# Kernel optimization log

Measured on AMD Instinct MI355X. Metric: run time of the kernel, lower is better.

## Reference

```python
import jax, jax.numpy as jnp
import numpy as np

NUM_LAYERS = 4; HEADS = 8; DIM_HEAD = 64; DIM = 512; FF_INNER = 2048; EPS = 1e-5
B = 32; S = 512
PAGE_VOCAB = 10000; ITEM_VOCAB = 100000; META_VOCAB = 1000
N_WIDE = 8; WIDE_DIM = 64
ATTN_INNER = HEADS * DIM_HEAD
FUSED = ATTN_INNER + DIM_HEAD + DIM_HEAD + 2 * FF_INNER  # q, k, v, swiglu-ff


def rotate_half(x):
    d = x.shape[-1] // 2
    x1, x2 = x[..., :d], x[..., d:]
    return jnp.concatenate([-x2, x1], axis=-1)


def rope_pos(n, d):
    inv_freq = 1.0 / (10000.0 ** (jnp.arange(0, d, 2, dtype=jnp.float32) / d))
    freqs = jnp.arange(n, dtype=jnp.float32)[:, None] * inv_freq[None, :]
    return jnp.concatenate([freqs, freqs], axis=-1)  # (n, d)


def wide_feat(w, bn_g, bn_b, W, bvec):
    # w: (B, n_wide, S); BatchNorm1d eval mode (running mean 0, var 1) -> affine only
    wn = w * (1.0 / np.sqrt(1.0 + EPS)) * bn_g[None, :, None] + bn_b[None, :, None]
    wt = jnp.transpose(wn, (0, 2, 1))  # (B, S, n_wide)
    return jax.nn.leaky_relu(wt @ W + bvec, negative_slope=0.2)


def parallel_block(x, vl, g, Wf, Wa, Wff):
    b, n, _ = x.shape
    mu = x.mean(-1, keepdims=True)
    var = ((x - mu) ** 2).mean(-1, keepdims=True)
    xn = (x - mu) / jnp.sqrt(var + EPS) * g  # gamma-only LayerNorm
    p = xn @ Wf  # (b, n, FUSED)
    q = p[..., :ATTN_INNER]
    k = p[..., ATTN_INNER:ATTN_INNER + DIM_HEAD]
    v = p[..., ATTN_INNER + DIM_HEAD:ATTN_INNER + 2 * DIM_HEAD]
    ff = p[..., ATTN_INNER + 2 * DIM_HEAD:]
    q = jnp.transpose(q.reshape(b, n, HEADS, DIM_HEAD), (0, 2, 1, 3))  # b h n d
    pos = rope_pos(n, DIM_HEAD)
    cos, sin = jnp.cos(pos), jnp.sin(pos)
    q = q * cos + rotate_half(q) * sin
    k = k * cos + rotate_half(k) * sin  # multi-query: k,v shared across heads
    q = q * (DIM_HEAD ** -0.5)
    sim = jnp.einsum('bhid,bjd->bhij', q, k)
    key_pad = jnp.arange(n)[None, :] >= vl[:, None]  # (b, n) True = padded key
    sim = jnp.where(key_pad[:, None, None, :], -jnp.inf, sim)
    attn = jax.nn.softmax(sim, axis=-1)
    out = jnp.einsum('bhij,bjd->bhid', attn, v)
    out = jnp.transpose(out, (0, 2, 1, 3)).reshape(b, n, ATTN_INNER)
    xx, gate = ff[..., :FF_INNER], ff[..., FF_INNER:]
    return out @ Wa + (jax.nn.silu(gate) * xx) @ Wff


def forward(page_in, item_in, item_meta_in, vl_in, page_meta_in,
            page_meta_wide_in, item_meta_wide_in,
            page_emb_table, page_meta_emb_table, item_emb_table,
            item_meta_emb_table, item_pre_emb_table,
            page_wide_W, page_wide_b, page_bn_g, page_bn_b,
            item_wide_W, item_wide_b, item_bn_g, item_bn_b,
            norm_g, fused_W, attn_out_W, ff_out_W):
    page_wide = wide_feat(page_meta_wide_in, page_bn_g, page_bn_b, page_wide_W, page_wide_b)
    item_wide = wide_feat(item_meta_wide_in, item_bn_g, item_bn_b, item_wide_W, item_wide_b)
    page = jnp.concatenate([page_emb_table[page_in], page_meta_emb_table[page_meta_in], page_wide], axis=-1)
    item = jnp.concatenate([item_emb_table[item_in], item_meta_emb_table[item_meta_in],
                            item_pre_emb_table[item_in], item_wide], axis=-1)
    x = page * item  # (B, S, DIM)
    for l in range(NUM_LAYERS):
        x = parallel_block(x, vl_in, norm_g[l], fused_W[l], attn_out_W[l], ff_out_W[l]) + x
    # MeanMaxPooling (dropout=0 in eval)
    return jnp.concatenate([x.mean(axis=1), x.max(axis=1)], axis=-1)  # (B, 2*DIM)


def setup_inputs() -> dict:
    key = jax.random.key(0)
    ks = jax.random.split(key, 24)
    s = 0.02
    return {
        'page_in': jax.random.randint(ks[0], (B, S), 0, PAGE_VOCAB),
        'item_in': jax.random.randint(ks[1], (B, S), 0, ITEM_VOCAB),
        'item_meta_in': jax.random.randint(ks[2], (B, S), 0, META_VOCAB),
        'vl_in': jax.random.randint(ks[3], (B,), 1, S + 1),
        'page_meta_in': jax.random.randint(ks[4], (B, S), 0, META_VOCAB),
        'page_meta_wide_in': jax.random.normal(ks[5], (B, N_WIDE, S), jnp.float32),
        'item_meta_wide_in': jax.random.normal(ks[6], (B, N_WIDE, S), jnp.float32),
        'page_emb_table': jax.random.normal(ks[7], (PAGE_VOCAB, 384), jnp.float32) * s,
        'page_meta_emb_table': jax.random.normal(ks[8], (META_VOCAB, 64), jnp.float32) * s,
        'item_emb_table': jax.random.normal(ks[9], (ITEM_VOCAB, 320), jnp.float32) * s,
        'item_meta_emb_table': jax.random.normal(ks[10], (META_VOCAB, 64), jnp.float32) * s,
        'item_pre_emb_table': jax.random.normal(ks[11], (ITEM_VOCAB, 64), jnp.float32) * s,
        'page_wide_W': jax.random.normal(ks[12], (N_WIDE, WIDE_DIM), jnp.float32) * s,
        'page_wide_b': jnp.zeros((WIDE_DIM,), jnp.float32),
        'page_bn_g': jnp.ones((N_WIDE,), jnp.float32),
        'page_bn_b': jnp.zeros((N_WIDE,), jnp.float32),
        'item_wide_W': jax.random.normal(ks[13], (N_WIDE, WIDE_DIM), jnp.float32) * s,
        'item_wide_b': jnp.zeros((WIDE_DIM,), jnp.float32),
        'item_bn_g': jnp.ones((N_WIDE,), jnp.float32),
        'item_bn_b': jnp.zeros((N_WIDE,), jnp.float32),
        'norm_g': jnp.ones((NUM_LAYERS, DIM), jnp.float32),
        'fused_W': jax.random.normal(ks[14], (NUM_LAYERS, DIM, FUSED), jnp.float32) * s,
        'attn_out_W': jax.random.normal(ks[15], (NUM_LAYERS, ATTN_INNER, DIM), jnp.float32) * s,
        'ff_out_W': jax.random.normal(ks[16], (NUM_LAYERS, FF_INNER, DIM), jnp.float32) * s,
    }


def reference(page_in, item_in, item_meta_in, vl_in, page_meta_in,
              page_meta_wide_in, item_meta_wide_in,
              page_emb_table, page_meta_emb_table, item_emb_table,
              item_meta_emb_table, item_pre_emb_table,
              page_wide_W, page_wide_b, page_bn_g, page_bn_b,
              item_wide_W, item_wide_b, item_bn_g, item_bn_b,
              norm_g, fused_W, attn_out_W, ff_out_W):
    return forward(page_in, item_in, item_meta_in, vl_in, page_meta_in,
                   page_meta_wide_in, item_meta_wide_in,
                   page_emb_table, page_meta_emb_table, item_emb_table,
                   item_meta_emb_table, item_pre_emb_table,
                   page_wide_W, page_wide_b, page_bn_g, page_bn_b,
                   item_wide_W, item_wide_b, item_bn_g, item_bn_b,
                   norm_g, fused_W, attn_out_W, ff_out_W)
```

## Files before the change

kernel.cpp:

```cpp
#include <hip/hip_runtime.h>
#include <math.h>


namespace {
constexpr int SEQ    = 512;
constexpr int NBATCH = 32;
constexpr int DIMM   = 512;
constexpr int NHEAD  = 8;
constexpr int FFIN   = 2048;
constexpr int NFUSED = 4736;
constexpr int NROWS  = NBATCH * SEQ;
constexpr int QKVC   = 640;
}

typedef __bf16 bf16x8 __attribute__((ext_vector_type(8)));
typedef float f32x4 __attribute__((ext_vector_type(4)));
typedef unsigned short ushort8 __attribute__((ext_vector_type(8)));

static __device__ __forceinline__ unsigned short bfhi(float v, float* hf) {
    __bf16 h = (__bf16)v;
    *hf = (float)h;
    return __builtin_bit_cast(unsigned short, h);
}
static __device__ __forceinline__ unsigned short bflo(float v, float hf) {
    __bf16 l = (__bf16)(v - hf);
    return __builtin_bit_cast(unsigned short, l);
}

static __device__ __forceinline__ void gload16(const unsigned short* g,
                                               unsigned short* l) {
    __builtin_amdgcn_global_load_lds(
        (const __attribute__((address_space(1))) void*)g,
        (__attribute__((address_space(3))) void*)l,
        16, 0, 0);
}

__global__ __launch_bounds__(512) void build_x_k(
    const int* __restrict__ page_in, const int* __restrict__ item_in,
    const int* __restrict__ item_meta_in, const int* __restrict__ page_meta_in,
    const float* __restrict__ pwide, const float* __restrict__ iwide,
    const float* __restrict__ page_emb, const float* __restrict__ page_meta_emb,
    const float* __restrict__ item_emb, const float* __restrict__ item_meta_emb,
    const float* __restrict__ item_pre_emb,
    const float* __restrict__ pW, const float* __restrict__ pb,
    const float* __restrict__ pg, const float* __restrict__ pbeta,
    const float* __restrict__ iW, const float* __restrict__ ib,
    const float* __restrict__ ig, const float* __restrict__ ibeta,
    float* __restrict__ x)
{
    const int row = blockIdx.x;
    const int b = row >> 9;
    const int s = row & 511;
    const int d = threadIdx.x;
    const float BNS = 0.9999950000374997f;

    float pv, iv;
    if (d < 384) {
        pv = page_emb[(size_t)page_in[row] * 384 + d];
    } else if (d < 448) {
        pv = page_meta_emb[(size_t)page_meta_in[row] * 64 + (d - 384)];
    } else {
        const int dd = d - 448;
        float acc = pb[dd];
        #pragma unroll
        for (int c = 0; c < 8; ++c) {
            float w  = pwide[((size_t)b * 8 + c) * SEQ + s];
            float wn = w * BNS * pg[c] + pbeta[c];
            acc += wn * pW[c * 64 + dd];
        }
        pv = acc > 0.f ? acc : 0.2f * acc;
    }
    if (d < 320) {
        iv = item_emb[(size_t)item_in[row] * 320 + d];
    } else if (d < 384) {
        iv = item_meta_emb[(size_t)item_meta_in[row] * 64 + (d - 320)];
    } else if (d < 448) {
        iv = item_pre_emb[(size_t)item_in[row] * 64 + (d - 384)];
    } else {
        const int dd = d - 448;
        float acc = ib[dd];
        #pragma unroll
        for (int c = 0; c < 8; ++c) {
            float w  = iwide[((size_t)b * 8 + c) * SEQ + s];
            float wn = w * BNS * ig[c] + ibeta[c];
            acc += wn * iW[c * 64 + dd];
        }
        iv = acc > 0.f ? acc : 0.2f * acc;
    }
    x[(size_t)row * DIMM + d] = pv * iv;
}

__global__ __launch_bounds__(256) void trig_k(float* __restrict__ cost,
                                              float* __restrict__ sint)
{
    const int idx = blockIdx.x * 256 + threadIdx.x;
    const int s = idx >> 5, j = idx & 31;
    float invf = powf(10000.0f, -(float)j * (1.0f / 32.0f));
    float ang = (float)s * invf;
    float sn, cs;
    sincosf(ang, &sn, &cs);
    cost[idx] = cs;
    sint[idx] = sn;
}

__global__ __launch_bounds__(256) void ln_k(const float* __restrict__ x,
                                            unsigned short* __restrict__ xnh,
                                            const float* __restrict__ g)
{
    const int row = blockIdx.x;
    const int t = threadIdx.x;
    const float* xr = x + (size_t)row * DIMM;
    __shared__ float red[4];

    float v0 = xr[t], v1 = xr[t + 256];
    float s = v0 + v1;
    #pragma unroll
    for (int o = 32; o; o >>= 1) s += __shfl_xor(s, o);
    if ((t & 63) == 0) red[t >> 6] = s;
    __syncthreads();
    float mu = (red[0] + red[1] + red[2] + red[3]) * (1.0f / 512.0f);
    __syncthreads();

    float d0 = v0 - mu, d1 = v1 - mu;
    float vs = d0 * d0 + d1 * d1;
    #pragma unroll
    for (int o = 32; o; o >>= 1) vs += __shfl_xor(vs, o);
    if ((t & 63) == 0) red[t >> 6] = vs;
    __syncthreads();
    float var = (red[0] + red[1] + red[2] + red[3]) * (1.0f / 512.0f);
    float r = 1.0f / sqrtf(var + 1e-5f);

    const size_t base = (size_t)row * DIMM;
    float o0 = d0 * r * g[t];
    float o1 = d1 * r * g[t + 256];
    float hf;
    xnh[base + t]       = bfhi(o0, &hf);
    xnh[base + t + 256] = bfhi(o1, &hf);
}

__global__ __launch_bounds__(256) void wconv_all_k(
    const float* __restrict__ Wf, const float* __restrict__ Wa,
    const float* __restrict__ Wff,
    unsigned short* __restrict__ WqTh, unsigned short* __restrict__ WqTl,
    unsigned short* __restrict__ WdTh, unsigned short* __restrict__ WaTh,
    unsigned short* __restrict__ WfTh)
{
    __shared__ float tile[64][65];
    const int bid = blockIdx.x;
    const int t   = threadIdx.x;

    const float* W;
    unsigned short* Th;
    unsigned short* Tl = nullptr;
    int ldw, col0, ldt, nt, kt;
    bool split = false;

    if (bid < 80) {
        W = Wf; ldw = NFUSED; col0 = 0; Th = WqTh; Tl = WqTl; ldt = DIMM;
        split = true;
        nt = bid % 10; kt = bid / 10;
    } else if (bid < 592) {
        int b = bid - 80;
        W = Wf; ldw = NFUSED; col0 = 640; Th = WdTh; ldt = DIMM;
        nt = b & 63; kt = b >> 6;
    } else if (bid < 656) {
        int b = bid - 592;
        W = Wa; ldw = DIMM; col0 = 0; Th = WaTh; ldt = DIMM;
        nt = b & 7; kt = b >> 3;
    } else {
        int b = bid - 656;
        W = Wff; ldw = DIMM; col0 = 0; Th = WfTh; ldt = FFIN;
        nt = b & 7; kt = b >> 3;
    }
    nt <<= 6; kt <<= 6;

    #pragma unroll
    for (int i = 0; i < 16; ++i) {
        int flat = i * 256 + t;
        int r = flat >> 6, c = flat & 63;
        tile[r][c] = W[(size_t)(kt + r) * ldw + col0 + nt + c];
    }
    __syncthreads();
    #pragma unroll
    for (int i = 0; i < 2; ++i) {
        int flat = i * 256 + t;
        int n = flat >> 3, ck = (flat & 7) << 3;
        ushort8 hv, lv;
        #pragma unroll
        for (int j = 0; j < 8; ++j) {
            float v = tile[ck + j][n];
            float hf;
            hv[j] = bfhi(v, &hf);
            if (split) lv[j] = bflo(v, hf);
        }
        size_t o = (size_t)(nt + n) * ldt + kt + ck;
        *(ushort8*)&Th[o] = hv;
        if (split) *(ushort8*)&Tl[o] = lv;
    }
}

__global__ __launch_bounds__(256, 4) void mfma_qkv_rope_k(
    const unsigned short* __restrict__ Ah,
    const unsigned short* __restrict__ BTh, const unsigned short* __restrict__ BTl,
    const float* __restrict__ cost, const float* __restrict__ sint,
    unsigned short* __restrict__ qh,
    unsigned short* __restrict__ kh, unsigned short* __restrict__ kl,
    unsigned short* __restrict__ vT)
{
    __shared__ unsigned short smem[128 * 64 + 64 * 64 + 64 * 64];
    unsigned short* sA  = smem;
    unsigned short* sBh = smem + 128 * 64;
    unsigned short* sBl = smem + 128 * 64 + 64 * 64;
    float* tileF = (float*)smem;

    const int n0 = blockIdx.x << 6;
    const int m0 = blockIdx.y << 7;
    const int t  = threadIdx.x;
    const int l  = t & 63;
    const int w  = t >> 6;
    const int wm = w >> 1, wn = w & 1;
    const int lr = l & 15, lg = l >> 4;
    const int lm = l >> 3;
    const int lc = l & 7;

    f32x4 acc[4][2];
    #pragma unroll
    for (int fm = 0; fm < 4; ++fm)
        #pragma unroll
        for (int fn = 0; fn < 2; ++fn) acc[fm][fn] = (f32x4)0.f;

    for (int k0 = 0; k0 < DIMM; k0 += 64) {
        __syncthreads();
        #pragma unroll
        for (int j = 0; j < 4; ++j) {
            int seg = w * 4 + j;
            int m = seg * 8 + lm;
            gload16(&Ah[(size_t)(m0 + m) * DIMM + k0 + ((lc ^ (m & 7)) << 3)],
                    &sA[seg * 512]);
        }
        #pragma unroll
        for (int j = 0; j < 2; ++j) {
            int seg = w * 2 + j;
            int n = seg * 8 + lm;
            int soff = (lc ^ (n & 7)) << 3;
            gload16(&BTh[(size_t)(n0 + n) * DIMM + k0 + soff], &sBh[seg * 512]);
            gload16(&BTl[(size_t)(n0 + n) * DIMM + k0 + soff], &sBl[seg * 512]);
        }
        __syncthreads();

        #pragma unroll
        for (int kk = 0; kk < 2; ++kk) {
            const int c = kk * 4 + lg;
            bf16x8 af[4];
            #pragma unroll
            for (int fm = 0; fm < 4; ++fm) {
                int m = wm * 64 + fm * 16 + lr;
                int lidx = m * 64 + ((c ^ (m & 7)) << 3);
                af[fm] = *(bf16x8*)&sA[lidx];
            }
            bf16x8 bh[2], bl[2];
            #pragma unroll
            for (int fn = 0; fn < 2; ++fn) {
                int n = wn * 32 + fn * 16 + lr;
                int lidx = n * 64 + ((c ^ (n & 7)) << 3);
                bh[fn] = *(bf16x8*)&sBh[lidx];
                bl[fn] = *(bf16x8*)&sBl[lidx];
            }
            #pragma unroll
            for (int fm = 0; fm < 4; ++fm)
                #pragma unroll
                for (int fn = 0; fn < 2; ++fn) {
                    acc[fm][fn] = __builtin_amdgcn_mfma_f32_16x16x32_bf16(af[fm], bh[fn], acc[fm][fn], 0, 0, 0);
                    acc[fm][fn] = __builtin_amdgcn_mfma_f32_16x16x32_bf16(af[fm], bl[fn], acc[fm][fn], 0, 0, 0);
                }
        }
    }

    __syncthreads();
    #pragma unroll
    for (int fm = 0; fm < 4; ++fm)
        #pragma unroll
        for (int fn = 0; fn < 2; ++fn) {
            const int nl = wn * 32 + fn * 16 + lr;
            #pragma unroll
            for (int r = 0; r < 4; ++r) {
                const int ml = wm * 64 + fm * 16 + lg * 4 + r;
                tileF[ml * 64 + ((nl + ml) & 63)] = acc[fm][fn][r];
            }
        }
    __syncthreads();

    const int tid = n0 >> 6;
    const int gb  = m0 >> 9;
    const int sb  = m0 & 511;

    if (tid < 8) {
        #pragma unroll 4
        for (int i = 0; i < 32; ++i) {
            int flat = i * 256 + t;
            int d = flat & 63, sl = flat >> 6;
            int s = sb + sl;
            float v  = tileF[sl * 64 + ((d + sl) & 63)];
            float vp = tileF[sl * 64 + (((d ^ 32) + sl) & 63)];
            float cs = cost[s * 32 + (d & 31)];
            float sn = sint[s * 32 + (d & 31)];
            float sgn = (d < 32) ? -1.f : 1.f;
            float o = (v * cs + sgn * vp * sn) * 0.125f;
            float hf;
            qh[(((size_t)gb * 8 + tid) * 512 + s) * 64 + d] = bfhi(o, &hf);
        }
    } else if (tid == 8) {
        #pragma unroll 4
        for (int i = 0; i < 32; ++i) {
            int flat = i * 256 + t;
            int d = flat & 63, sl = flat >> 6;
            int s = sb + sl;
            float v  = tileF[sl * 64 + ((d + sl) & 63)];
            float vp = tileF[sl * 64 + (((d ^ 32) + sl) & 63)];
            float cs = cost[s * 32 + (d & 31)];
            float sn = sint[s * 32 + (d & 31)];
            float sgn = (d < 32) ? -1.f : 1.f;
            float o = v * cs + sgn * vp * sn;
            float hf;
            size_t idx = ((size_t)gb * 512 + s) * 64 + d;
            kh[idx] = bfhi(o, &hf);
            kl[idx] = bflo(o, hf);
        }
    } else {
        #pragma unroll 4
        for (int i = 0; i < 32; ++i) {
            int flat = i * 256 + t;
            int sl = flat & 127, d = flat >> 7;
            float v = tileF[sl * 64 + ((d + sl) & 63)];
            float hf;
            vT[((size_t)gb * 64 + d) * 512 + sb + sl] = bfhi(v, &hf);
        }
    }
}

__global__ __launch_bounds__(256, 2) void mfma_out_k(
    const unsigned short* __restrict__ A1,
    const unsigned short* __restrict__ B1,
    const unsigned short* __restrict__ A2,
    const unsigned short* __restrict__ B2,
    float* __restrict__ X)
{
    __shared__ unsigned short sA[64 * 64];
    __shared__ unsigned short sB[256 * 64];

    const int bid = blockIdx.x;
    const int swz = (bid & 7) * 64 + (bid >> 3);
    const int n0 = (swz & 1) << 8;
    const int m0 = (swz >> 1) << 6;

    const int t  = threadIdx.x;
    const int l  = t & 63;
    const int w  = t >> 6;
    const int lr = l & 15, lg = l >> 4;
    const int lm = l >> 3;
    const int lc = l & 7;

    f32x4 acc[4][4];
    #pragma unroll
    for (int fm = 0; fm < 4; ++fm)
        #pragma unroll
        for (int fn = 0; fn < 4; ++fn) acc[fm][fn] = (f32x4)0.f;

    #pragma unroll
    for (int pass = 0; pass < 2; ++pass) {
        const unsigned short* pA = pass ? A2 : A1;
        const unsigned short* pB = pass ? B2 : B1;
        const int lda = pass ? FFIN : DIMM;
        const int KK  = pass ? FFIN : DIMM;

        for (int k0 = 0; k0 < KK; k0 += 64) {
            __syncthreads();
            #pragma unroll
            for (int j = 0; j < 2; ++j) {
                int seg = w * 2 + j;
                int m = seg * 8 + lm;
                gload16(&pA[(size_t)(m0 + m) * lda + k0 + ((lc ^ (m & 7)) << 3)],
                        &sA[seg * 512]);
            }
            #pragma unroll
            for (int j = 0; j < 8; ++j) {
                int seg = w * 8 + j;
                int n = seg * 8 + lm;
                gload16(&pB[(size_t)(n0 + n) * KK + k0 + ((lc ^ (n & 7)) << 3)],
                        &sB[seg * 512]);
            }
            __syncthreads();

            #pragma unroll
            for (int kk = 0; kk < 2; ++kk) {
                const int c = kk * 4 + lg;
                bf16x8 af[4];
                #pragma unroll
                for (int fm = 0; fm < 4; ++fm) {
                    int m = fm * 16 + lr;
                    int lidx = m * 64 + ((c ^ (m & 7)) << 3);
                    af[fm] = *(bf16x8*)&sA[lidx];
                }
                bf16x8 bfr[4];
                #pragma unroll
                for (int fn = 0; fn < 4; ++fn) {
                    int n = w * 64 + fn * 16 + lr;
                    int lidx = n * 64 + ((c ^ (n & 7)) << 3);
                    bfr[fn] = *(bf16x8*)&sB[lidx];
                }
                #pragma unroll
                for (int fm = 0; fm < 4; ++fm)
                    #pragma unroll
                    for (int fn = 0; fn < 4; ++fn)
                        acc[fm][fn] = __builtin_amdgcn_mfma_f32_16x16x32_bf16(af[fm], bfr[fn], acc[fm][fn], 0, 0, 0);
            }
        }
    }

    #pragma unroll
    for (int fm = 0; fm < 4; ++fm)
        #pragma unroll
        for (int fn = 0; fn < 4; ++fn) {
            const int n = n0 + w * 64 + fn * 16 + lr;
            #pragma unroll
            for (int r = 0; r < 4; ++r) {
                const int m = m0 + fm * 16 + lg * 4 + r;
                X[(size_t)m * DIMM + n] += acc[fm][fn][r];
            }
        }
}

__global__ __launch_bounds__(256, 4) void mfma_dual_silu_k(
    const unsigned short* __restrict__ Ah,
    const unsigned short* __restrict__ WTh,
    unsigned short* __restrict__ Hh)
{
    __shared__ unsigned short sA[128 * 64];
    __shared__ unsigned short sBx[64 * 64];
    __shared__ unsigned short sBg[64 * 64];

    const int n0 = blockIdx.x << 6;
    const int m0 = blockIdx.y << 7;
    const int t  = threadIdx.x;
    const int l  = t & 63;
    const int w  = t >> 6;
    const int wm = w >> 1, wn = w & 1;
    const int lr = l & 15, lg = l >> 4;
    const int lm = l >> 3;
    const int lc = l & 7;

    f32x4 accX[4][2], accG[4][2];
    #pragma unroll
    for (int fm = 0; fm < 4; ++fm)
        #pragma unroll
        for (int fn = 0; fn < 2; ++fn) {
            accX[fm][fn] = (f32x4)0.f;
            accG[fm][fn] = (f32x4)0.f;
        }

    for (int k0 = 0; k0 < DIMM; k0 += 64) {
        __syncthreads();
        #pragma unroll
        for (int j = 0; j < 4; ++j) {
            int seg = w * 4 + j;
            int m = seg * 8 + lm;
            gload16(&Ah[(size_t)(m0 + m) * DIMM + k0 + ((lc ^ (m & 7)) << 3)],
                    &sA[seg * 512]);
        }
        #pragma unroll
        for (int j = 0; j < 2; ++j) {
            int seg = w * 2 + j;
            int n = seg * 8 + lm;
            int soff = (lc ^ (n & 7)) << 3;
            gload16(&WTh[(size_t)(n0 + n) * DIMM + k0 + soff], &sBx[seg * 512]);
            gload16(&WTh[(size_t)(2048 + n0 + n) * DIMM + k0 + soff], &sBg[seg * 512]);
        }
        __syncthreads();

        #pragma unroll
        for (int kk = 0; kk < 2; ++kk) {
            const int c = kk * 4 + lg;
            bf16x8 af[4];
            #pragma unroll
            for (int fm = 0; fm < 4; ++fm) {
                int m = wm * 64 + fm * 16 + lr;
                int lidx = m * 64 + ((c ^ (m & 7)) << 3);
                af[fm] = *(bf16x8*)&sA[lidx];
            }
            bf16x8 bx[2], bg[2];
            #pragma unroll
            for (int fn = 0; fn < 2; ++fn) {
                int n = wn * 32 + fn * 16 + lr;
                int lidx = n * 64 + ((c ^ (n & 7)) << 3);
                bx[fn] = *(bf16x8*)&sBx[lidx];
                bg[fn] = *(bf16x8*)&sBg[lidx];
            }
            #pragma unroll
            for (int fm = 0; fm < 4; ++fm)
                #pragma unroll
                for (int fn = 0; fn < 2; ++fn) {
                    accX[fm][fn] = __builtin_amdgcn_mfma_f32_16x16x32_bf16(af[fm], bx[fn], accX[fm][fn], 0, 0, 0);
                    accG[fm][fn] = __builtin_amdgcn_mfma_f32_16x16x32_bf16(af[fm], bg[fn], accG[fm][fn], 0, 0, 0);
                }
        }
    }

    __syncthreads();
    #pragma unroll
    for (int fm = 0; fm < 4; ++fm)
        #pragma unroll
        for (int fn = 0; fn < 2; ++fn) {
            const int nl = wn * 32 + fn * 16 + lr;
            const int cc = nl >> 3;
            #pragma unroll
            for (int r = 0; r < 4; ++r) {
                const int ml = wm * 64 + fm * 16 + lg * 4 + r;
                float gv = accG[fm][fn][r];
                float xv = accX[fm][fn][r];
                float sig = 1.0f / (1.0f + __expf(-gv));
                float hv = gv * sig * xv;
                float hf;
                sA[ml * 64 + ((cc ^ (ml & 7)) << 3) + (nl & 7)] = bfhi(hv, &hf);
            }
        }
    __syncthreads();
    #pragma unroll
    for (int i = 0; i < 4; ++i) {
        int flat = i * 256 + t;
        int m = flat >> 3, c = flat & 7;
        ushort8 v = *(ushort8*)&sA[m * 64 + ((c ^ (m & 7)) << 3)];
        __builtin_nontemporal_store(v, (ushort8*)&Hh[(size_t)(m0 + m) * FFIN + n0 + c * 8]);
    }
}

__global__ __launch_bounds__(256) void attn_mfma_k(
    const unsigned short* __restrict__ qh,
    const unsigned short* __restrict__ kh, const unsigned short* __restrict__ kl,
    const unsigned short* __restrict__ vT,
    unsigned short* __restrict__ ctxh,
    const int* __restrict__ vl)
{
    __shared__ unsigned short sKh[64 * 64];
    __shared__ unsigned short sKl[64 * 64];
    __shared__ unsigned short sVT[64 * 64];
    __shared__ unsigned short sP[64 * 64];

    const int i0 = blockIdx.x << 6;
    const int h  = blockIdx.y;
    const int b  = blockIdx.z;
    const int t  = threadIdx.x;
    const int l  = t & 63;
    const int w  = t >> 6;
    const int lr = l & 15, lg = l >> 4;
    const int VL = vl[b];
    const int ntiles = (VL + 63) >> 6;

    bf16x8 qfh[2];
    {
        size_t base = (((size_t)(b * 8 + h) * 512) + i0 + w * 16 + lr) * 64 + lg * 8;
        qfh[0] = *(const bf16x8*)&qh[base];
        qfh[1] = *(const bf16x8*)&qh[base + 32];
    }

    float mrow[4], lrow[4];
    f32x4 oacc[4];
    #pragma unroll
    for (int r = 0; r < 4; ++r) { mrow[r] = -3.0e38f; lrow[r] = 0.f; }
    #pragma unroll
    for (int nb = 0; nb < 4; ++nb) oacc[nb] = (f32x4)0.f;

    for (int jt = 0; jt < ntiles; ++jt) {
        const int j0 = jt << 6;
        __syncthreads();
        #pragma unroll
        for (int i = 0; i < 2; ++i) {
            int flat = i * 256 + t;
            int m = flat >> 3, c = flat & 7;
            int lidx = m * 64 + ((c ^ (m & 7)) << 3);
            size_t kg = ((size_t)b * 512 + j0 + m) * 64 + c * 8;
            *(ushort8*)&sKh[lidx] = *(const ushort8*)&kh[kg];
            *(ushort8*)&sKl[lidx] = *(const ushort8*)&kl[kg];
            size_t vg = ((size_t)b * 64 + m) * 512 + j0 + c * 8;
            *(ushort8*)&sVT[lidx] = *(const ushort8*)&vT[vg];
        }
        __syncthreads();

        f32x4 accS[4];
        #pragma unroll
        for (int nb = 0; nb < 4; ++nb) accS[nb] = (f32x4)0.f;
        #pragma unroll
        for (int ks = 0; ks < 2; ++ks) {
            const int c = ks * 4 + lg;
            #pragma unroll
            for (int nb = 0; nb < 4; ++nb) {
                int n = nb * 16 + lr;
                int lidx = n * 64 + ((c ^ (n & 7)) << 3);
                bf16x8 kfh = *(bf16x8*)&sKh[lidx];
                bf16x8 kfl = *(bf16x8*)&sKl[lidx];
                accS[nb] = __builtin_amdgcn_mfma_f32_16x16x32_bf16(qfh[ks], kfh, accS[nb], 0, 0, 0);
                accS[nb] = __builtin_amdgcn_mfma_f32_16x16x32_bf16(qfh[ks], kfl, accS[nb], 0, 0, 0);
            }
        }

        #pragma unroll
        for (int nb = 0; nb < 4; ++nb) {
            if (j0 + nb * 16 + lr >= VL) {
                #pragma unroll
                for (int r = 0; r < 4; ++r) accS[nb][r] = -3.0e38f;
            }
        }

        #pragma unroll
        for (int r = 0; r < 4; ++r) {
            float rm = fmaxf(fmaxf(accS[0][r], accS[1][r]), fmaxf(accS[2][r], accS[3][r]));
            #pragma unroll
            for (int off = 8; off; off >>= 1) rm = fmaxf(rm, __shfl_xor(rm, off));
            float nm = fmaxf(mrow[r], rm);
            float scl = __expf(mrow[r] - nm);
            mrow[r] = nm;
            float ps = 0.f;
            #pragma unroll
            for (int nb = 0; nb < 4; ++nb) {
                float p = __expf(accS[nb][r] - nm);
                accS[nb][r] = p;
                ps += p;
            }
            lrow[r] = lrow[r] * scl + ps;
            #pragma unroll
            for (int nb = 0; nb < 4; ++nb) oacc[nb][r] *= scl;
        }

        #pragma unroll
        for (int nb = 0; nb < 4; ++nb) {
            int cc = nb * 2 + (lr >> 3);
            #pragma unroll
            for (int r = 0; r < 4; ++r) {
                int q = w * 16 + lg * 4 + r;
                int lidx = q * 64 + ((cc ^ (q & 7)) << 3) + (lr & 7);
                float hf2;
                sP[lidx] = bfhi(accS[nb][r], &hf2);
            }
        }

        #pragma unroll
        for (int ks = 0; ks < 2; ++ks) {
            const int c = ks * 4 + lg;
            int qrow = w * 16 + lr;
            int plidx = qrow * 64 + ((c ^ (qrow & 7)) << 3);
            bf16x8 pf = *(bf16x8*)&sP[plidx];
            #pragma unroll
            for (int nb = 0; nb < 4; ++nb) {
                int n = nb * 16 + lr;
                int lidx = n * 64 + ((c ^ (n & 7)) << 3);
                bf16x8 vf = *(bf16x8*)&sVT[lidx];
                oacc[nb] = __builtin_amdgcn_mfma_f32_16x16x32_bf16(pf, vf, oacc[nb], 0, 0, 0);
            }
        }
    }

    #pragma unroll
    for (int r = 0; r < 4; ++r) {
        float lt = lrow[r];
        #pragma unroll
        for (int off = 8; off; off >>= 1) lt += __shfl_xor(lt, off);
        float inv = 1.0f / lt;
        const int row = (b << 9) + i0 + w * 16 + lg * 4 + r;
        const size_t base = (size_t)row * DIMM + h * 64;
        #pragma unroll
        for (int nb = 0; nb < 4; ++nb) {
            float v = oacc[nb][r] * inv;
            float hf;
            ctxh[base + nb * 16 + lr] = bfhi(v, &hf);
        }
    }
}

__global__ __launch_bounds__(512) void pool_part_k(const float* __restrict__ x,
                                                   float* __restrict__ psum,
                                                   float* __restrict__ pmax)
{
    const int seg = blockIdx.x;
    const int b   = blockIdx.y;
    const int d   = threadIdx.x;
    const float* xb = x + ((size_t)(b << 9) + (seg << 6)) * DIMM;
    float s = 0.f, m = -3.0e38f;
    for (int i = 0; i < 64; ++i) {
        float v = xb[(size_t)i * DIMM + d];
        s += v;
        m = fmaxf(m, v);
    }
    psum[((size_t)b * 8 + seg) * DIMM + d] = s;
    pmax[((size_t)b * 8 + seg) * DIMM + d] = m;
}

__global__ __launch_bounds__(512) void pool_comb_k(const float* __restrict__ psum,
                                                   const float* __restrict__ pmax,
                                                   float* __restrict__ out)
{
    const int b = blockIdx.x;
    const int d = threadIdx.x;
    float s = 0.f, m = -3.0e38f;
    #pragma unroll
    for (int seg = 0; seg < 8; ++seg) {
        s += psum[((size_t)b * 8 + seg) * DIMM + d];
        m = fmaxf(m, pmax[((size_t)b * 8 + seg) * DIMM + d]);
    }
    out[b * 1024 + d] = s * (1.0f / 512.0f);
    out[b * 1024 + 512 + d] = m;
}

extern "C" void kernel_launch(void* const* d_in, const int* in_sizes, int n_in,
                              void* d_out, int out_size, void* d_ws, size_t ws_size,
                              hipStream_t stream)
{
    const int*   page_in        = (const int*)d_in[0];
    const int*   item_in        = (const int*)d_in[1];
    const int*   item_meta_in   = (const int*)d_in[2];
    const int*   vl_in          = (const int*)d_in[3];
    const int*   page_meta_in   = (const int*)d_in[4];
    const float* pwide          = (const float*)d_in[5];
    const float* iwide          = (const float*)d_in[6];
    const float* page_emb       = (const float*)d_in[7];
    const float* page_meta_emb  = (const float*)d_in[8];
    const float* item_emb       = (const float*)d_in[9];
    const float* item_meta_emb  = (const float*)d_in[10];
    const float* item_pre_emb   = (const float*)d_in[11];
    const float* pW             = (const float*)d_in[12];
    const float* pb             = (const float*)d_in[13];
    const float* pg             = (const float*)d_in[14];
    const float* pbeta          = (const float*)d_in[15];
    const float* iW             = (const float*)d_in[16];
    const float* ib             = (const float*)d_in[17];
    const float* ig             = (const float*)d_in[18];
    const float* ibeta          = (const float*)d_in[19];
    const float* norm_g         = (const float*)d_in[20];
    const float* fused_W        = (const float*)d_in[21];
    const float* attn_out_W     = (const float*)d_in[22];
    const float* ff_out_W       = (const float*)d_in[23];
    float* out = (float*)d_out;

    float* ws  = (float*)d_ws;
    float* x    = ws;
    unsigned short* xnh = (unsigned short*)(x + (size_t)NROWS * DIMM);
    unsigned short* qhb = xnh + (size_t)NROWS * DIMM;
    unsigned short* hh   = qhb + (size_t)NROWS * DIMM;
    unsigned short* ctxh = hh + (size_t)NROWS * FFIN;
    float* psum = (float*)(ctxh + (size_t)NROWS * DIMM);
    float* pmax = psum + (size_t)NBATCH * 8 * DIMM;
    unsigned short* WqTh = (unsigned short*)(pmax + (size_t)NBATCH * 8 * DIMM);
    unsigned short* WqTl = WqTh + (size_t)QKVC * DIMM;
    unsigned short* WdTh = WqTl + (size_t)QKVC * DIMM;
    unsigned short* WaTh = WdTh + (size_t)4096 * DIMM;
    unsigned short* WfTh = WaTh + (size_t)DIMM * DIMM;
    unsigned short* khb  = WfTh + (size_t)DIMM * FFIN;
    unsigned short* klb  = khb + (size_t)NBATCH * SEQ * 64;
    unsigned short* vTb  = klb + (size_t)NBATCH * SEQ * 64;
    float* cost = (float*)(vTb + (size_t)NBATCH * 64 * SEQ);
    float* sint = cost + 512 * 32;

    build_x_k<<<NROWS, 512, 0, stream>>>(
        page_in, item_in, item_meta_in, page_meta_in, pwide, iwide,
        page_emb, page_meta_emb, item_emb, item_meta_emb, item_pre_emb,
        pW, pb, pg, pbeta, iW, ib, ig, ibeta, x);

    trig_k<<<64, 256, 0, stream>>>(cost, sint);

    for (int l = 0; l < 4; ++l) {
        const float* Wf  = fused_W    + (size_t)l * DIMM * NFUSED;
        const float* Wa  = attn_out_W + (size_t)l * DIMM * DIMM;
        const float* Wff = ff_out_W   + (size_t)l * FFIN * DIMM;
        const float* g   = norm_g     + (size_t)l * DIMM;

        ln_k<<<NROWS, 256, 0, stream>>>(x, xnh, g);

        wconv_all_k<<<912, 256, 0, stream>>>(
            Wf, Wa, Wff, WqTh, WqTl, WdTh, WaTh, WfTh);

        mfma_qkv_rope_k<<<dim3(QKVC / 64, NROWS / 128), 256, 0, stream>>>(
            xnh, WqTh, WqTl, cost, sint, qhb, khb, klb, vTb);

        mfma_dual_silu_k<<<dim3(FFIN / 64, NROWS / 128), 256, 0, stream>>>(
            xnh, WdTh, hh);

        attn_mfma_k<<<dim3(SEQ / 64, NHEAD, NBATCH), 256, 0, stream>>>(
            qhb, khb, klb, vTb, ctxh, vl_in);

        mfma_out_k<<<512, 256, 0, stream>>>(
            ctxh, WaTh, hh, WfTh, x);
    }

    pool_part_k<<<dim3(8, NBATCH), 512, 0, stream>>>(x, psum, pmax);
    pool_comb_k<<<NBATCH, 512, 0, stream>>>(psum, pmax, out);
}
```

Measured before the change: 962.6 us.

## Double-buffer LDS tiles in output projection GEMM to overlap loads with MFMA

The output-projection GEMM kernel, which fuses attention-out and FF-out, now uses two LDS buffers. The next K tile is issued with async global-to-LDS loads while the current tile is computed, and explicit vmcnt waits plus barriers replace the per-tile double syncthreads. This is meant to hide global memory latency behind MFMA work. LDS usage roughly doubles (about 80KB per block), which may reduce occupancy below the declared launch bound of 2 blocks per CU.

```diff
diff --git a/kernel.cpp b/kernel.cpp
--- a/kernel.cpp
+++ b/kernel.cpp
@@ -345,8 +345,8 @@
     const unsigned short* __restrict__ B2,
     float* __restrict__ X)
 {
-    __shared__ unsigned short sA[64 * 64];
-    __shared__ unsigned short sB[256 * 64];
+    __shared__ unsigned short sA[2][64 * 64];
+    __shared__ unsigned short sB[2][256 * 64];
 
     const int bid = blockIdx.x;
     const int swz = (bid & 7) * 64 + (bid >> 3);
@@ -366,56 +366,72 @@
         #pragma unroll
         for (int fn = 0; fn < 4; ++fn) acc[fm][fn] = (f32x4)0.f;
 
-    #pragma unroll
-    for (int pass = 0; pass < 2; ++pass) {
-        const unsigned short* pA = pass ? A2 : A1;
-        const unsigned short* pB = pass ? B2 : B1;
-        const int lda = pass ? FFIN : DIMM;
-        const int KK  = pass ? FFIN : DIMM;
-
-        for (int k0 = 0; k0 < KK; k0 += 64) {
-            __syncthreads();
-            #pragma unroll
-            for (int j = 0; j < 2; ++j) {
-                int seg = w * 2 + j;
-                int m = seg * 8 + lm;
-                gload16(&pA[(size_t)(m0 + m) * lda + k0 + ((lc ^ (m & 7)) << 3)],
-                        &sA[seg * 512]);
-            }
-            #pragma unroll
-            for (int j = 0; j < 8; ++j) {
-                int seg = w * 8 + j;
-                int n = seg * 8 + lm;
-                gload16(&pB[(size_t)(n0 + n) * KK + k0 + ((lc ^ (n & 7)) << 3)],
-                        &sB[seg * 512]);
-            }
-            __syncthreads();
-
-            #pragma unroll
-            for (int kk = 0; kk < 2; ++kk) {
-                const int c = kk * 4 + lg;
-                bf16x8 af[4];
+    auto stage = [&](int buf, int tt) {
+        const unsigned short* pA = (tt < 8) ? A1 : A2;
+        const unsigned short* pB = (tt < 8) ? B1 : B2;
+        const int lda = (tt < 8) ? DIMM : FFIN;
+        const int KK  = (tt < 8) ? DIMM : FFIN;
+        const int k0  = ((tt < 8) ? tt : tt - 8) << 6;
+        #pragma unroll
+        for (int j = 0; j < 2; ++j) {
+            int seg = w * 2 + j;
+            int m = seg * 8 + lm;
+            gload16(&pA[(size_t)(m0 + m) * lda + k0 + ((lc ^ (m & 7)) << 3)],
+                    &sA[buf][seg * 512]);
+        }
+        #pragma unroll
+        for (int j = 0; j < 8; ++j) {
+            int seg = w * 8 + j;
+            int n = seg * 8 + lm;
+            gload16(&pB[(size_t)(n0 + n) * KK + k0 + ((lc ^ (n & 7)) << 3)],
+                    &sB[buf][seg * 512]);
+        }
+    };
+
+    auto compute = [&](int buf) {
+        #pragma unroll
+        for (int kk = 0; kk < 2; ++kk) {
+            const int c = kk * 4 + lg;
+            bf16x8 af[4];
+            #pragma unroll
+            for (int fm = 0; fm < 4; ++fm) {
+                int m = fm * 16 + lr;
+                int lidx = m * 64 + ((c ^ (m & 7)) << 3);
+                af[fm] = *(bf16x8*)&sA[buf][lidx];
+            }
+            bf16x8 bfr[4];
+            #pragma unroll
+            for (int fn = 0; fn < 4; ++fn) {
+                int n = w * 64 + fn * 16 + lr;
+                int lidx = n * 64 + ((c ^ (n & 7)) << 3);
+                bfr[fn] = *(bf16x8*)&sB[buf][lidx];
+            }
+            #pragma unroll
+            for (int fm = 0; fm < 4; ++fm)
                 #pragma unroll
-                for (int fm = 0; fm < 4; ++fm) {
-                    int m = fm * 16 + lr;
-                    int lidx = m * 64 + ((c ^ (m & 7)) << 3);
-                    af[fm] = *(bf16x8*)&sA[lidx];
-                }
-                bf16x8 bfr[4];
-                #pragma unroll
-                for (int fn = 0; fn < 4; ++fn) {
-                    int n = w * 64 + fn * 16 + lr;
-                    int lidx = n * 64 + ((c ^ (n & 7)) << 3);
-                    bfr[fn] = *(bf16x8*)&sB[lidx];
-                }
-                #pragma unroll
-                for (int fm = 0; fm < 4; ++fm)
-                    #pragma unroll
-                    for (int fn = 0; fn < 4; ++fn)
-                        acc[fm][fn] = __builtin_amdgcn_mfma_f32_16x16x32_bf16(af[fm], bfr[fn], acc[fm][fn], 0, 0, 0);
-            }
-        }
-    }
+                for (int fn = 0; fn < 4; ++fn)
+                    acc[fm][fn] = __builtin_amdgcn_mfma_f32_16x16x32_bf16(af[fm], bfr[fn], acc[fm][fn], 0, 0, 0);
+        }
+    };
+
+    stage(0, 0);
+    asm volatile("s_waitcnt vmcnt(0)" ::: "memory");
+    __builtin_amdgcn_sched_barrier(0);
+    __builtin_amdgcn_s_barrier();
+    int cur = 0;
+    for (int tt = 0; tt < 39; ++tt) {
+        stage(cur ^ 1, tt + 1);
+        asm volatile("s_waitcnt vmcnt(10)" ::: "memory");
+        __builtin_amdgcn_sched_barrier(0);
+        __builtin_amdgcn_s_barrier();
+        compute(cur);
+        __builtin_amdgcn_s_barrier();
+        cur ^= 1;
+    }
+    asm volatile("s_waitcnt vmcnt(0)" ::: "memory");
+    __builtin_amdgcn_sched_barrier(0);
+    __builtin_amdgcn_s_barrier();
+    compute(cur);
 
     #pragma unroll
     for (int fm = 0; fm < 4; ++fm)
```

Result: no change. 949.8 us (-1.3%).
